# Optimization experiments

Hardware: AMD Instinct MI355X
Metric: run time of the kernel (lower is better)

The kernel has to match this reference:

```python
import jax, jax.numpy as jnp
import numpy as np

B, S, D, H = 2, 4096, 768, 12
DK = D // H


def setup_inputs() -> dict:
    key = jax.random.key(0)
    ks = jax.random.split(key, 12)
    inp = {
        "q": jax.random.normal(ks[0], (B, S, D), dtype=jnp.float32),
        "k": jax.random.normal(ks[1], (B, S, D), dtype=jnp.float32),
        "v": jax.random.normal(ks[2], (B, S, D), dtype=jnp.float32),
        "mask": jax.random.randint(ks[3], (B, 1, 1, S), 0, 2, dtype=jnp.int32),
        "w_q": jax.random.normal(ks[4], (D, D), dtype=jnp.float32) * 0.02,
        "b_q": jnp.zeros((D,), dtype=jnp.float32),
        "w_k": jax.random.normal(ks[5], (D, D), dtype=jnp.float32) * 0.02,
        "b_k": jnp.zeros((D,), dtype=jnp.float32),
        "w_v": jax.random.normal(ks[6], (D, D), dtype=jnp.float32) * 0.02,
        "b_v": jnp.zeros((D,), dtype=jnp.float32),
        "w_o": jax.random.normal(ks[7], (D, D), dtype=jnp.float32) * 0.02,
        "b_o": jnp.zeros((D,), dtype=jnp.float32),
    }
    return inp


def reference(q, k, v, mask, w_q, b_q, w_k, b_k, w_v, b_v, w_o, b_o):
    scale = 1.0 / jnp.sqrt(jnp.asarray(DK, dtype=q.dtype))
    # projections, then split heads: [B, S, H, DK]
    Q = (q @ w_q + b_q).reshape(B, S, H, DK)
    K = (k @ w_k + b_k).reshape(B, S, H, DK)
    V = (v @ w_v + b_v).reshape(B, S, H, DK)
    # scores: [B, H, Sq, Sk]
    scores = jnp.einsum("bqhd,bkhd->bhqk", Q, K) * scale
    scores = jnp.where(mask == 0, jnp.asarray(-1e9, dtype=scores.dtype), scores)
    attn = jax.nn.softmax(scores, axis=-1)
    # dropout prob is 0.0 (eval): identity
    out = jnp.einsum("bhqk,bkhd->bqhd", attn, V).reshape(B, S, D)
    return out @ w_o + b_o
```

## Files before the change

kernel.cpp:

```cpp
#include <hip/hip_runtime.h>
#include <hip/hip_fp16.h>
#include <stdint.h>

typedef _Float16 hf;
typedef hf hfx8 __attribute__((ext_vector_type(8)));
typedef hf hfx2 __attribute__((ext_vector_type(2)));
typedef float f32x4 __attribute__((ext_vector_type(4)));

constexpr int CB  = 2;
constexpr int CS  = 4096;
constexpr int CD  = 768;
constexpr int CH  = 12;
constexpr int CDK = 64;
constexpr int CBH = CB * CH;
constexpr int CM  = CB * CS;
constexpr float CS_SCALE = 0.18033688f;

__device__ __forceinline__ void gload16(const void* g, void* l) {
  __builtin_amdgcn_global_load_lds((const __attribute__((address_space(1))) void*)g,
                                   (__attribute__((address_space(3))) void*)l, 16, 0, 0);
}

__global__ __launch_bounds__(256) void k_convert3(const float* __restrict__ q, const float* __restrict__ k,
                                                  const float* __restrict__ v,
                                                  hf* __restrict__ qo, hf* __restrict__ ko,
                                                  hf* __restrict__ vo, int n8) {
  const float* in; hf* out;
  if      (blockIdx.y == 0) { in = q; out = qo; }
  else if (blockIdx.y == 1) { in = k; out = ko; }
  else                      { in = v; out = vo; }
  int i = blockIdx.x * 256 + threadIdx.x;
  if (i >= n8) return;
  const float4* p = (const float4*)in;
  float4 a = p[i * 2], b = p[i * 2 + 1];
  hfx8 o;
  o[0] = (hf)a.x; o[1] = (hf)a.y; o[2] = (hf)a.z; o[3] = (hf)a.w;
  o[4] = (hf)b.x; o[5] = (hf)b.y; o[6] = (hf)b.z; o[7] = (hf)b.w;
  ((hfx8*)out)[i] = o;
}

__global__ __launch_bounds__(256) void k_wtrans(const float* __restrict__ w0, const float* __restrict__ w1,
                                                const float* __restrict__ w2, const float* __restrict__ w3,
                                                hf* __restrict__ o0, hf* __restrict__ o1,
                                                hf* __restrict__ o2, hf* __restrict__ o3) {
  const float* w; hf* o;
  float sc = 1.f;
  if      (blockIdx.z == 0) { w = w0; o = o0; sc = CS_SCALE; }
  else if (blockIdx.z == 1) { w = w1; o = o1; }
  else if (blockIdx.z == 2) { w = w2; o = o2; }
  else                      { w = w3; o = o3; }
  __shared__ float t[32][33];
  int k0 = blockIdx.x * 32, n0 = blockIdx.y * 32;
  int tx = threadIdx.x & 31, ty = threadIdx.x >> 5;
#pragma unroll
  for (int i = 0; i < 4; ++i) {
    int kk = ty + i * 8;
    t[kk][tx] = w[(size_t)(k0 + kk) * CD + n0 + tx];
  }
  __syncthreads();
#pragma unroll
  for (int i = 0; i < 4; ++i) {
    int nn = ty + i * 8;
    o[(size_t)(n0 + nn) * CD + k0 + tx] = (hf)(t[tx][nn] * sc);
  }
}

template <int EPI, int BN>
__device__ __forceinline__ void gemm_core(const hf* __restrict__ A, const hf* __restrict__ Bt,
                                          const float* __restrict__ bias, float bsc,
                                          void* __restrict__ outp,
                                          int K, int mtile, int ntile) {
  constexpr int WC = BN / 64;
  constexpr int WR = 4 / WC;
  constexpr int MI = 128 / (16 * WR);
  __shared__ hf As[2][128 * 32];
  __shared__ hf Bs[2][BN * 32];
  const int tid = threadIdx.x;
  const int lane = tid & 63;
  const int wid = tid >> 6;
  const int wr = wid / WC, wc = wid % WC;
  const int r = lane & 15, g = lane >> 4;
  const int m0 = mtile * 128, n0 = ntile * BN;

  f32x4 acc[MI][4] = {};

  auto stageAB = [&](int bsel, int kt) {
#pragma unroll
    for (int i = 0; i < 2; ++i) {
      int flat = tid * 8 + i * 2048;
      int rr = flat >> 5, cc = flat & 31;
      gload16(A + (size_t)(m0 + rr) * K + kt + cc, (char*)&As[bsel][0] + (size_t)flat * 2);
    }
#pragma unroll
    for (int i = 0; i < BN / 64; ++i) {
      int flat = tid * 8 + i * 2048;
      int rr = flat >> 5, cc = flat & 31;
      gload16(Bt + (size_t)(n0 + rr) * K + kt + cc, (char*)&Bs[bsel][0] + (size_t)flat * 2);
    }
  };

  stageAB(0, 0);
  const int NKT = K / 32;
  for (int t = 0; t < NKT; ++t) {
    __syncthreads();
    if (t + 1 < NKT) stageAB((t + 1) & 1, (t + 1) * 32);
    const hf* Asb = &As[t & 1][0];
    const hf* Bsb = &Bs[t & 1][0];

    hfx8 af[MI], bfr[4];
#pragma unroll
    for (int mi = 0; mi < MI; ++mi)
      af[mi] = *(const hfx8*)(Asb + (wr * (MI * 16) + mi * 16 + r) * 32 + g * 8);
#pragma unroll
    for (int ni = 0; ni < 4; ++ni)
      bfr[ni] = *(const hfx8*)(Bsb + (wc * 64 + ni * 16 + r) * 32 + g * 8);
    __builtin_amdgcn_s_setprio(1);
#pragma unroll
    for (int mi = 0; mi < MI; ++mi)
#pragma unroll
      for (int ni = 0; ni < 4; ++ni)
        acc[mi][ni] = __builtin_amdgcn_mfma_f32_16x16x32_f16(af[mi], bfr[ni], acc[mi][ni], 0, 0, 0);
    __builtin_amdgcn_s_setprio(0);
  }

  if (EPI == 0) {
    hf* o = (hf*)outp;
#pragma unroll
    for (int ni = 0; ni < 4; ++ni) {
      int col = n0 + wc * 64 + ni * 16 + r;
      float bv = bias[col] * bsc;
      int h = col >> 6, dk = col & 63;
#pragma unroll
      for (int mi = 0; mi < MI; ++mi) {
#pragma unroll
        for (int q = 0; q < 4; ++q) {
          int row = m0 + wr * (MI * 16) + mi * 16 + g * 4 + q;
          int b = row >> 12, s = row & 4095;
          o[(size_t)((b * CH + h) * CS + s) * CDK + dk] = (hf)(acc[mi][ni][q] + bv);
        }
      }
    }
  } else {
    float* o = (float*)outp;
#pragma unroll
    for (int ni = 0; ni < 4; ++ni) {
      int col = n0 + wc * 64 + ni * 16 + r;
      float bv = bias[col];
#pragma unroll
      for (int mi = 0; mi < MI; ++mi) {
#pragma unroll
        for (int q = 0; q < 4; ++q) {
          int row = m0 + wr * (MI * 16) + mi * 16 + g * 4 + q;
          o[(size_t)row * CD + col] = acc[mi][ni][q] + bv;
        }
      }
    }
  }
}

__global__ __launch_bounds__(256) void k_qkv(const hf* __restrict__ qb, const hf* __restrict__ kb,
                                             const hf* __restrict__ vb,
                                             const hf* __restrict__ wqT, const hf* __restrict__ wkT,
                                             const hf* __restrict__ wvT,
                                             const float* __restrict__ bq, const float* __restrict__ bk,
                                             const float* __restrict__ bv,
                                             hf* __restrict__ Qh, hf* __restrict__ Kh,
                                             hf* __restrict__ Vh) {
  const hf* A; const hf* W; const float* bias; hf* O; float bsc = 1.f;
  if      (blockIdx.z == 0) { A = qb; W = wqT; bias = bq; O = Qh; bsc = CS_SCALE; }
  else if (blockIdx.z == 1) { A = kb; W = wkT; bias = bk; O = Kh; }
  else                      { A = vb; W = wvT; bias = bv; O = Vh; }
  gemm_core<0, 128>(A, W, bias, bsc, O, CD, blockIdx.x, blockIdx.y);
}

__global__ __launch_bounds__(256) void k_out(const hf* __restrict__ ao, const hf* __restrict__ woT,
                                             const float* __restrict__ bo, float* __restrict__ out) {
  gemm_core<1, 64>(ao, woT, bo, 1.f, out, CD, blockIdx.x, blockIdx.y);
}

__global__ __launch_bounds__(256) void k_scan(const int* __restrict__ mask, int* __restrict__ idx,
                                              int* __restrict__ nk) {
  int b = blockIdx.x;
  const int* m = mask + b * CS;
  int tid = threadIdx.x, lane = tid & 63, wv = tid >> 6;
  int base = tid * 16;
  int mv[16];
  const int4* m4 = (const int4*)(m + base);
#pragma unroll
  for (int i = 0; i < 4; ++i) {
    int4 x = m4[i];
    mv[i * 4 + 0] = x.x; mv[i * 4 + 1] = x.y; mv[i * 4 + 2] = x.z; mv[i * 4 + 3] = x.w;
  }
  int local = 0;
#pragma unroll
  for (int j = 0; j < 16; ++j) local += (mv[j] != 0);
  int pre = local;
#pragma unroll
  for (int d = 1; d < 64; d <<= 1) {
    int t = __shfl_up(pre, d, 64);
    if (lane >= d) pre += t;
  }
  __shared__ int wsum[4];
  if (lane == 63) wsum[wv] = pre;
  __syncthreads();
  int woff = 0;
  for (int w = 0; w < wv; ++w) woff += wsum[w];
  int pos = woff + pre - local;
  int* ib = idx + b * CS;
#pragma unroll
  for (int j = 0; j < 16; ++j)
    if (mv[j]) ib[pos++] = base + j;
  if (tid == 255) nk[b] = woff + pre;
}

__global__ __launch_bounds__(256) void k_gather(const hf* __restrict__ Kh, const hf* __restrict__ Vh,
                                                const int* __restrict__ idx, const int* __restrict__ nk,
                                                hf* __restrict__ Kc, hf* __restrict__ VTc) {
  int bh = blockIdx.y, b = bh / CH;
  int nkb = nk[b];
  int nkp = (nkb + 63) & ~63;
  int i0 = blockIdx.x * 64;
  if (i0 >= nkp) return;
  const int* ib = idx + b * CS;
  int tid = threadIdx.x;
  __shared__ hf t[64][72];
#pragma unroll
  for (int i = 0; i < 2; ++i) {
    int f = tid + i * 256;
    int ii = f >> 3, c8 = (f & 7) << 3;
    int gi = i0 + ii;
    hfx8 kv = {}, vv = {};
    if (gi < nkb) {
      int s = ib[gi];
      kv = *(const hfx8*)&Kh[((size_t)bh * CS + s) * CDK + c8];
      vv = *(const hfx8*)&Vh[((size_t)bh * CS + s) * CDK + c8];
    }
    *(hfx8*)&Kc[((size_t)bh * CS + gi) * CDK + c8] = kv;
#pragma unroll
    for (int j = 0; j < 8; ++j) t[ii][c8 + j] = vv[j];
  }
  __syncthreads();
#pragma unroll
  for (int i = 0; i < 2; ++i) {
    int f = tid + i * 256;
    int d = f >> 3, s8 = (f & 7) << 3;
    hfx8 vv;
#pragma unroll
    for (int j = 0; j < 8; ++j) vv[j] = t[s8 + j][d];
    *(hfx8*)&VTc[((size_t)bh * CDK + d) * CS + i0 + s8] = vv;
  }
}

__device__ __forceinline__ int KSWZ(int key) { return ((key & 3) + ((key >> 3) & 1) * 4) << 4; }

__global__ __launch_bounds__(256) void k_attn(const hf* __restrict__ Qh, const hf* __restrict__ Kc,
                                              const hf* __restrict__ VTc, const int* __restrict__ nk,
                                              hf* __restrict__ attn_out) {
  __shared__ hf Ks[2][64 * 64];
  __shared__ hf VTs[2][64 * 64];

  const int tid = threadIdx.x;
  const int lane = tid & 63, wv = tid >> 6;
  const int r = lane & 15, g = lane >> 4;
  const int bh = blockIdx.y;
  const int b = bh / CH, h = bh % CH;
  const int q0 = blockIdx.x * 128 + wv * 32;
  const int nkb = nk[b];
  const int ntiles = (nkb + 63) >> 6;

  hfx8 aq[2][2];
#pragma unroll
  for (int rg = 0; rg < 2; ++rg) {
    size_t qrow = (size_t)bh * CS + q0 + rg * 16 + r;
    aq[rg][0] = *(const hfx8*)&Qh[qrow * CDK + g * 8];
    aq[rg][1] = *(const hfx8*)&Qh[qrow * CDK + 32 + g * 8];
  }

  hfx8 ones;
#pragma unroll
  for (int j = 0; j < 8; ++j) ones[j] = (hf)1.f;

  f32x4 accO[2][4] = {};
  f32x4 l_acc[2] = {};

  auto stage = [&](int bsel, int kt) {
    char* KsB0 = (char*)&Ks[bsel][0];
    char* VTsB0 = (char*)&VTs[bsel][0];
#pragma unroll
    for (int i = 0; i < 2; ++i) {
      int f = tid + i * 256;
      int row = f >> 3, sl = f & 7;
      int srcb = (sl * 16) ^ KSWZ(row);
      gload16(Kc + (size_t)(bh * CS + kt + row) * CDK + (srcb >> 1), KsB0 + (size_t)f * 16);
    }
#pragma unroll
    for (int i = 0; i < 2; ++i) {
      int f = tid + i * 256;
      int row = f >> 3, sl = f & 7;
      int srcb = (sl * 16) ^ ((row & 7) << 4);
      gload16(VTc + (size_t)(bh * CDK + row) * CS + kt + (srcb >> 1), VTsB0 + (size_t)f * 16);
    }
  };

  stage(0, 0);

  for (int t = 0; t < ntiles; ++t) {
    __syncthreads();
    if (t + 1 < ntiles) stage((t + 1) & 1, (t + 1) * 64);
    const int kt = t * 64;
    char* KsB = (char*)&Ks[t & 1][0];
    char* VTsB = (char*)&VTs[t & 1][0];
    const bool tail = (kt + 64 > nkb);

    f32x4 s[2][4] = {};
    __builtin_amdgcn_s_setprio(1);
#pragma unroll
    for (int kb = 0; kb < 4; ++kb) {
      const int key = 8 * (r >> 2) + 32 * (kb >> 1) + 4 * (kb & 1) + (r & 3);
#pragma unroll
      for (int kh = 0; kh < 2; ++kh) {
        int byteoff = key * 128 + ((kh * 64 + g * 16) ^ KSWZ(key));
        hfx8 ka = *(const hfx8*)(KsB + byteoff);
        s[0][kb] = __builtin_amdgcn_mfma_f32_16x16x32_f16(ka, aq[0][kh], s[0][kb], 0, 0, 0);
        s[1][kb] = __builtin_amdgcn_mfma_f32_16x16x32_f16(ka, aq[1][kh], s[1][kb], 0, 0, 0);
      }
    }
    __builtin_amdgcn_s_setprio(0);

    union PK { hfx2 h2[8]; hfx8 v[2]; };
    PK pk[2];
#pragma unroll
    for (int rg = 0; rg < 2; ++rg) {
      if (tail) {
#pragma unroll
        for (int kb = 0; kb < 4; ++kb)
#pragma unroll
          for (int q = 0; q < 4; ++q)
            if (kt + 8 * g + 32 * (kb >> 1) + 4 * (kb & 1) + q >= nkb) s[rg][kb][q] = -1024.f;
      }
#pragma unroll
      for (int kb = 0; kb < 4; ++kb) {
        hfx2 a = __builtin_bit_cast(hfx2, __builtin_amdgcn_cvt_pkrtz(s[rg][kb][0], s[rg][kb][1]));
        hfx2 c = __builtin_bit_cast(hfx2, __builtin_amdgcn_cvt_pkrtz(s[rg][kb][2], s[rg][kb][3]));
        pk[rg].h2[kb * 2 + 0] = __builtin_elementwise_exp2(a);
        pk[rg].h2[kb * 2 + 1] = __builtin_elementwise_exp2(c);
      }
    }

    __builtin_amdgcn_s_setprio(1);
#pragma unroll
    for (int kh = 0; kh < 2; ++kh) {
      l_acc[0] = __builtin_amdgcn_mfma_f32_16x16x32_f16(pk[0].v[kh], ones, l_acc[0], 0, 0, 0);
      l_acc[1] = __builtin_amdgcn_mfma_f32_16x16x32_f16(pk[1].v[kh], ones, l_acc[1], 0, 0, 0);
    }
#pragma unroll
    for (int nb = 0; nb < 4; ++nb) {
#pragma unroll
      for (int kh = 0; kh < 2; ++kh) {
        int d = nb * 16 + r;
        int byteoff = d * 128 + ((kh * 64 + g * 16) ^ ((d & 7) << 4));
        hfx8 bvf = *(const hfx8*)(VTsB + byteoff);
        accO[0][nb] = __builtin_amdgcn_mfma_f32_16x16x32_f16(pk[0].v[kh], bvf, accO[0][nb], 0, 0, 0);
        accO[1][nb] = __builtin_amdgcn_mfma_f32_16x16x32_f16(pk[1].v[kh], bvf, accO[1][nb], 0, 0, 0);
      }
    }
    __builtin_amdgcn_s_setprio(0);
  }

#pragma unroll
  for (int rg = 0; rg < 2; ++rg) {
#pragma unroll
    for (int q = 0; q < 4; ++q) {
      float inv = 1.f / l_acc[rg][q];
      int srow = q0 + rg * 16 + g * 4 + q;
      size_t bs = (size_t)b * CS + srow;
#pragma unroll
      for (int nb = 0; nb < 4; ++nb) {
        int d = nb * 16 + r;
        attn_out[bs * CD + h * 64 + d] = (hf)(accO[rg][nb][q] * inv);
      }
    }
  }
}

extern "C" void kernel_launch(void* const* d_in, const int* in_sizes, int n_in,
                              void* d_out, int out_size, void* d_ws, size_t ws_size,
                              hipStream_t stream) {
  const float* q   = (const float*)d_in[0];
  const float* k   = (const float*)d_in[1];
  const float* v   = (const float*)d_in[2];
  const int*  mask = (const int*)d_in[3];
  const float* w_q = (const float*)d_in[4];
  const float* b_q = (const float*)d_in[5];
  const float* w_k = (const float*)d_in[6];
  const float* b_k = (const float*)d_in[7];
  const float* w_v = (const float*)d_in[8];
  const float* b_v = (const float*)d_in[9];
  const float* w_o = (const float*)d_in[10];
  const float* b_o = (const float*)d_in[11];

  char* ws = (char*)d_ws;
  size_t off = 0;
  auto alloc = [&](size_t bytes) { char* p = ws + off; off += (bytes + 255) & ~255ULL; return p; };

  const size_t MD2 = (size_t)CM * CD * 2;
  const size_t WT2 = (size_t)CD * CD * 2;
  hf* qb  = (hf*)alloc(MD2);
  hf* kb  = (hf*)alloc(MD2);
  hf* vb  = (hf*)alloc(MD2);
  hf* wqT = (hf*)alloc(WT2);
  hf* wkT = (hf*)alloc(WT2);
  hf* wvT = (hf*)alloc(WT2);
  hf* woT = (hf*)alloc(WT2);
  hf* Qh  = (hf*)alloc(MD2);
  hf* Kh  = (hf*)alloc(MD2);
  hf* Vh  = (hf*)alloc(MD2);
  int* idx = (int*)alloc((size_t)CB * CS * 4);
  int* nkd = (int*)alloc(256);
  hf* Kc  = qb;
  hf* VTc = kb;
  hf* ao  = vb;
  (void)ws_size; (void)in_sizes; (void)n_in; (void)out_size;

  const int n8 = CM * CD / 8;
  dim3 blk(256);

  k_convert3<<<dim3((n8 + 255) / 256, 3), blk, 0, stream>>>(q, k, v, qb, kb, vb, n8);
  k_wtrans<<<dim3(CD / 32, CD / 32, 4), blk, 0, stream>>>(w_q, w_k, w_v, w_o, wqT, wkT, wvT, woT);
  k_scan<<<dim3(CB), blk, 0, stream>>>(mask, idx, nkd);
  k_qkv<<<dim3(CM / 128, CD / 128, 3), blk, 0, stream>>>(qb, kb, vb, wqT, wkT, wvT, b_q, b_k, b_v, Qh, Kh, Vh);
  k_gather<<<dim3(CS / 64, CBH), blk, 0, stream>>>(Kh, Vh, idx, nkd, Kc, VTc);
  k_attn<<<dim3(CS / 128, CBH), blk, 0, stream>>>(Qh, Kc, VTc, nkd, ao);
  k_out<<<dim3(CM / 128, CD / 64), blk, 0, stream>>>(ao, woT, b_o, (float*)d_out);
}
```

Before: 166.8 us.

## Fuse key/value compaction into QKV GEMM epilogue, drop gather kernel

The mask scan now writes an inverse index (compacted position or -1) per key, and the K and V projection epilogues scatter results directly into the compacted K and transposed V buffers, skipping masked rows. This removes the separate gather/transpose kernel and the full-size Kh/Vh intermediate round trip through memory. A small zero-pad kernel fills the tail up to a multiple of 64. The transposed V epilogue writes are strided and uncoalesced, and separately the attention kernel now preloads all V fragments from LDS before the softmax exp to overlap LDS latency, at the cost of more registers.

```diff
diff --git a/kernel.cpp b/kernel.cpp
--- a/kernel.cpp
+++ b/kernel.cpp
@@ -68,7 +68,7 @@
 template <int EPI, int BN>
 __device__ __forceinline__ void gemm_core(const hf* __restrict__ A, const hf* __restrict__ Bt,
                                           const float* __restrict__ bias, float bsc,
-                                          void* __restrict__ outp,
+                                          void* __restrict__ outp, const int* __restrict__ inv,
                                           int K, int mtile, int ntile) {
   constexpr int WC = BN / 64;
   constexpr int WR = 4 / WC;
@@ -140,7 +140,7 @@
         }
       }
     }
-  } else {
+  } else if (EPI == 1) {
     float* o = (float*)outp;
 #pragma unroll
     for (int ni = 0; ni < 4; ++ni) {
@@ -152,6 +152,28 @@
         for (int q = 0; q < 4; ++q) {
           int row = m0 + wr * (MI * 16) + mi * 16 + g * 4 + q;
           o[(size_t)row * CD + col] = acc[mi][ni][q] + bv;
+        }
+      }
+    }
+  } else {
+    hf* o = (hf*)outp;
+#pragma unroll
+    for (int mi = 0; mi < MI; ++mi) {
+#pragma unroll
+      for (int q = 0; q < 4; ++q) {
+        int row = m0 + wr * (MI * 16) + mi * 16 + g * 4 + q;
+        int b = row >> 12, s = row & 4095;
+        int pos = inv[b * CS + s];
+        if (pos < 0) continue;
+#pragma unroll
+        for (int ni = 0; ni < 4; ++ni) {
+          int col = n0 + wc * 64 + ni * 16 + r;
+          float bv = bias[col];
+          int h = col >> 6, dk = col & 63;
+          size_t bh = (size_t)(b * CH + h);
+          hf val = (hf)(acc[mi][ni][q] + bv);
+          if (EPI == 2) o[(bh * CS + pos) * CDK + dk] = val;
+          else          o[(bh * CDK + dk) * CS + pos] = val;
         }
       }
     }
@@ -164,21 +186,23 @@
                                              const hf* __restrict__ wvT,
                                              const float* __restrict__ bq, const float* __restrict__ bk,
                                              const float* __restrict__ bv,
-                                             hf* __restrict__ Qh, hf* __restrict__ Kh,
-                                             hf* __restrict__ Vh) {
-  const hf* A; const hf* W; const float* bias; hf* O; float bsc = 1.f;
-  if      (blockIdx.z == 0) { A = qb; W = wqT; bias = bq; O = Qh; bsc = CS_SCALE; }
-  else if (blockIdx.z == 1) { A = kb; W = wkT; bias = bk; O = Kh; }
-  else                      { A = vb; W = wvT; bias = bv; O = Vh; }
-  gemm_core<0, 128>(A, W, bias, bsc, O, CD, blockIdx.x, blockIdx.y);
+                                             const int* __restrict__ inv,
+                                             hf* __restrict__ Qh, hf* __restrict__ Kc,
+                                             hf* __restrict__ VTc) {
+  if (blockIdx.z == 0)
+    gemm_core<0, 128>(qb, wqT, bq, CS_SCALE, Qh, nullptr, CD, blockIdx.x, blockIdx.y);
+  else if (blockIdx.z == 1)
+    gemm_core<2, 128>(kb, wkT, bk, 1.f, Kc, inv, CD, blockIdx.x, blockIdx.y);
+  else
+    gemm_core<3, 128>(vb, wvT, bv, 1.f, VTc, inv, CD, blockIdx.x, blockIdx.y);
 }
 
 __global__ __launch_bounds__(256) void k_out(const hf* __restrict__ ao, const hf* __restrict__ woT,
                                              const float* __restrict__ bo, float* __restrict__ out) {
-  gemm_core<1, 64>(ao, woT, bo, 1.f, out, CD, blockIdx.x, blockIdx.y);
-}
-
-__global__ __launch_bounds__(256) void k_scan(const int* __restrict__ mask, int* __restrict__ idx,
+  gemm_core<1, 64>(ao, woT, bo, 1.f, out, nullptr, CD, blockIdx.x, blockIdx.y);
+}
+
+__global__ __launch_bounds__(256) void k_scan(const int* __restrict__ mask, int* __restrict__ inv,
                                               int* __restrict__ nk) {
   int b = blockIdx.x;
   const int* m = mask + b * CS;
@@ -206,48 +230,28 @@
   int woff = 0;
   for (int w = 0; w < wv; ++w) woff += wsum[w];
   int pos = woff + pre - local;
-  int* ib = idx + b * CS;
+  int* ib = inv + b * CS;
 #pragma unroll
   for (int j = 0; j < 16; ++j)
-    if (mv[j]) ib[pos++] = base + j;
+    ib[base + j] = mv[j] ? pos++ : -1;
   if (tid == 255) nk[b] = woff + pre;
 }
 
-__global__ __launch_bounds__(256) void k_gather(const hf* __restrict__ Kh, const hf* __restrict__ Vh,
-                                                const int* __restrict__ idx, const int* __restrict__ nk,
-                                                hf* __restrict__ Kc, hf* __restrict__ VTc) {
-  int bh = blockIdx.y, b = bh / CH;
+__global__ __launch_bounds__(256) void k_zeropad(const int* __restrict__ nk,
+                                                 hf* __restrict__ Kc, hf* __restrict__ VTc) {
+  int bh = blockIdx.x, b = bh / CH;
   int nkb = nk[b];
   int nkp = (nkb + 63) & ~63;
-  int i0 = blockIdx.x * 64;
-  if (i0 >= nkp) return;
-  const int* ib = idx + b * CS;
+  int npad = nkp - nkb;
+  if (npad == 0) return;
   int tid = threadIdx.x;
-  __shared__ hf t[64][72];
-#pragma unroll
-  for (int i = 0; i < 2; ++i) {
-    int f = tid + i * 256;
-    int ii = f >> 3, c8 = (f & 7) << 3;
-    int gi = i0 + ii;
-    hfx8 kv = {}, vv = {};
-    if (gi < nkb) {
-      int s = ib[gi];
-      kv = *(const hfx8*)&Kh[((size_t)bh * CS + s) * CDK + c8];
-      vv = *(const hfx8*)&Vh[((size_t)bh * CS + s) * CDK + c8];
-    }
-    *(hfx8*)&Kc[((size_t)bh * CS + gi) * CDK + c8] = kv;
-#pragma unroll
-    for (int j = 0; j < 8; ++j) t[ii][c8 + j] = vv[j];
-  }
-  __syncthreads();
-#pragma unroll
-  for (int i = 0; i < 2; ++i) {
-    int f = tid + i * 256;
-    int d = f >> 3, s8 = (f & 7) << 3;
-    hfx8 vv;
-#pragma unroll
-    for (int j = 0; j < 8; ++j) vv[j] = t[s8 + j][d];
-    *(hfx8*)&VTc[((size_t)bh * CDK + d) * CS + i0 + s8] = vv;
+  for (int i = tid; i < npad * 64; i += 256) {
+    int rr = i / 64, cc = i - rr * 64;
+    Kc[((size_t)bh * CS + nkb + rr) * CDK + cc] = (hf)0.f;
+  }
+  for (int i = tid; i < 64 * npad; i += 256) {
+    int d = i / npad, cc = i - d * npad;
+    VTc[((size_t)bh * CDK + d) * CS + nkb + cc] = (hf)0.f;
   }
 }
 
@@ -327,6 +331,17 @@
     }
     __builtin_amdgcn_s_setprio(0);
 
+    hfx8 bvf[4][2];
+#pragma unroll
+    for (int nb = 0; nb < 4; ++nb) {
+#pragma unroll
+      for (int kh = 0; kh < 2; ++kh) {
+        int d = nb * 16 + r;
+        int byteoff = d * 128 + ((kh * 64 + g * 16) ^ ((d & 7) << 4));
+        bvf[nb][kh] = *(const hfx8*)(VTsB + byteoff);
+      }
+    }
+
     union PK { hfx2 h2[8]; hfx8 v[2]; };
     PK pk[2];
 #pragma unroll
@@ -357,11 +372,8 @@
     for (int nb = 0; nb < 4; ++nb) {
 #pragma unroll
       for (int kh = 0; kh < 2; ++kh) {
-        int d = nb * 16 + r;
-        int byteoff = d * 128 + ((kh * 64 + g * 16) ^ ((d & 7) << 4));
-        hfx8 bvf = *(const hfx8*)(VTsB + byteoff);
-        accO[0][nb] = __builtin_amdgcn_mfma_f32_16x16x32_f16(pk[0].v[kh], bvf, accO[0][nb], 0, 0, 0);
-        accO[1][nb] = __builtin_amdgcn_mfma_f32_16x16x32_f16(pk[1].v[kh], bvf, accO[1][nb], 0, 0, 0);
+        accO[0][nb] = __builtin_amdgcn_mfma_f32_16x16x32_f16(pk[0].v[kh], bvf[nb][kh], accO[0][nb], 0, 0, 0);
+        accO[1][nb] = __builtin_amdgcn_mfma_f32_16x16x32_f16(pk[1].v[kh], bvf[nb][kh], accO[1][nb], 0, 0, 0);
       }
     }
     __builtin_amdgcn_s_setprio(0);
@@ -413,13 +425,11 @@
   hf* wvT = (hf*)alloc(WT2);
   hf* woT = (hf*)alloc(WT2);
   hf* Qh  = (hf*)alloc(MD2);
-  hf* Kh  = (hf*)alloc(MD2);
-  hf* Vh  = (hf*)alloc(MD2);
-  int* idx = (int*)alloc((size_t)CB * CS * 4);
+  hf* Kc  = (hf*)alloc(MD2);
+  hf* VTc = (hf*)alloc(MD2);
+  int* inv = (int*)alloc((size_t)CB * CS * 4);
   int* nkd = (int*)alloc(256);
-  hf* Kc  = qb;
-  hf* VTc = kb;
-  hf* ao  = vb;
+  hf* ao  = qb;
   (void)ws_size; (void)in_sizes; (void)n_in; (void)out_size;
 
   const int n8 = CM * CD / 8;
@@ -427,9 +437,9 @@
 
   k_convert3<<<dim3((n8 + 255) / 256, 3), blk, 0, stream>>>(q, k, v, qb, kb, vb, n8);
   k_wtrans<<<dim3(CD / 32, CD / 32, 4), blk, 0, stream>>>(w_q, w_k, w_v, w_o, wqT, wkT, wvT, woT);
-  k_scan<<<dim3(CB), blk, 0, stream>>>(mask, idx, nkd);
-  k_qkv<<<dim3(CM / 128, CD / 128, 3), blk, 0, stream>>>(qb, kb, vb, wqT, wkT, wvT, b_q, b_k, b_v, Qh, Kh, Vh);
-  k_gather<<<dim3(CS / 64, CBH), blk, 0, stream>>>(Kh, Vh, idx, nkd, Kc, VTc);
+  k_scan<<<dim3(CB), blk, 0, stream>>>(mask, inv, nkd);
+  k_zeropad<<<dim3(CBH), blk, 0, stream>>>(nkd, Kc, VTc);
+  k_qkv<<<dim3(CM / 128, CD / 128, 3), blk, 0, stream>>>(qb, kb, vb, wqT, wkT, wvT, b_q, b_k, b_v, inv, Qh, Kc, VTc);
   k_attn<<<dim3(CS / 128, CBH), blk, 0, stream>>>(Qh, Kc, VTc, nkd, ao);
   k_out<<<dim3(CM / 128, CD / 64), blk, 0, stream>>>(ao, woT, b_o, (float*)d_out);
 }
```

After: 226.7 us. 1.36x slower.
